# Performance work log

Hardware: AMD Instinct MI355X
Metric: run time of the kernel (lower is better)

The kernel has to match this reference:

```python
import jax, jax.numpy as jnp
import numpy as np

B, S, E, H = 2, 2048, 1024, 16
D = E // H
LN_EPS = 1e-5
NORM_EPS = 1e-12  # F.normalize clamp_min


def setup_inputs() -> dict:
    key = jax.random.key(0)
    ks = jax.random.split(key, 4)
    x = jax.random.normal(ks[0], (B, S, E), dtype=jnp.float32)
    qkv_w = jax.random.normal(ks[1], (3 * E, E), dtype=jnp.float32) * 0.02
    qkv_b = jnp.zeros((3 * E,), dtype=jnp.float32)
    out_w = jax.random.normal(ks[2], (E, E), dtype=jnp.float32) * 0.02
    out_b = jnp.zeros((E,), dtype=jnp.float32)
    ln_w = jnp.ones((E,), dtype=jnp.float32)
    ln_b = jnp.zeros((E,), dtype=jnp.float32)
    qknorm_scale = jnp.asarray(E ** -0.5, dtype=jnp.float32)
    # RotaryEmbedding buffer: inv_freq interleaved (emb[::2] = emb[1::2] = base**(-arange(0,E,2)/E))
    base_freq = 10000.0 ** (-(np.arange(0, E, 2).astype(np.float32) / E))
    emb = np.empty((E,), dtype=np.float32)
    emb[::2] = base_freq
    emb[1::2] = base_freq
    inv_freq = jnp.asarray(emb)
    return {"x": x, "ln_w": ln_w, "ln_b": ln_b, "qkv_w": qkv_w, "qkv_b": qkv_b,
            "qknorm_scale": qknorm_scale, "out_w": out_w, "out_b": out_b, "inv_freq": inv_freq}


def _rotate(t, sin, cos):
    # Faithful to source: x1 = even idx (excluding last), x2 = odd idx; cat(-x2, x1)
    x1 = t[..., :-1:2]
    x2 = t[..., 1::2]
    t_rot = jnp.concatenate((-x2, x1), axis=-1)
    return t * cos + t_rot * sin


def _l2norm(t):
    n = jnp.sqrt(jnp.sum(t * t, axis=-1, keepdims=True))
    return t / jnp.maximum(n, NORM_EPS)


def reference(x, ln_w, ln_b, qkv_w, qkv_b, qknorm_scale, out_w, out_b, inv_freq):
    # --- prenorm (LayerNorm, eps=1e-5) ---
    mu = jnp.mean(x, axis=-1, keepdims=True)
    var = jnp.mean((x - mu) ** 2, axis=-1, keepdims=True)
    xn = (x - mu) / jnp.sqrt(var + LN_EPS) * ln_w + ln_b
    # --- QKV projection ---
    qkv = xn @ qkv_w.T + qkv_b  # [B,S,3E]
    q, k, v = jnp.split(qkv, 3, axis=-1)
    # --- rotary (source uses scalar seq*inv_freq, not per-position) ---
    seq = q.shape[1]
    sin = jnp.sin(seq * inv_freq)
    cos = jnp.cos(seq * inv_freq)
    q = _rotate(q, sin, cos)
    k = _rotate(k, sin, cos)
    # --- split heads: [B,S,E] -> [B,H,S,D] ---
    split = lambda t: t.reshape(B, seq, H, D).transpose(0, 2, 1, 3)
    q, k, v = split(q), split(k), split(v)
    # --- qknorm ---
    q = _l2norm(q) * qknorm_scale
    k = _l2norm(k) * qknorm_scale
    # --- scaled dot product with causal mask ---
    aw = jnp.einsum('bhqd,bhkd->bhqk', q, k)  # [B,H,S,S]
    causal = jnp.tril(jnp.ones((seq, seq), dtype=bool))
    aw = jnp.where(causal, aw, jnp.finfo(aw.dtype).min)
    aw = jax.nn.softmax(aw, axis=-1)
    attn = jnp.einsum('bhqk,bhkd->bhqd', aw, v)
    # --- merge heads + out proj ---
    attn = attn.transpose(0, 2, 1, 3).reshape(B, seq, E)
    return attn @ out_w.T + out_b
```

## Files before the change

kernel.cpp:

```cpp
#include <hip/hip_runtime.h>

typedef unsigned short u16;
typedef __attribute__((ext_vector_type(8))) short bf16x8;
typedef __attribute__((ext_vector_type(4))) float f32x4;

#define SS 2048
#define EE 1024
#define HH 16
#define DD 64

__device__ __forceinline__ float b2f(u16 u) {
  union { unsigned int i; float f; } v; v.i = ((unsigned int)u) << 16; return v.f;
}
__device__ __forceinline__ u16 f2b(float f) {
  union { float f; unsigned int i; } v; v.f = f;
  unsigned int i = v.i;
  return (u16)((i + 0x7FFFu + ((i >> 16) & 1u)) >> 16);
}

#define GLD16(g, l)                                                         \
  __builtin_amdgcn_global_load_lds(                                         \
      (const __attribute__((address_space(1))) unsigned int*)(g),           \
      (__attribute__((address_space(3))) unsigned int*)(l), 16, 0, 0)

__global__ __launch_bounds__(256) void k_prep(const float* __restrict__ qkv_w,
                                              u16* __restrict__ wq_b,
                                              const float* __restrict__ inv_freq,
                                              float2* __restrict__ cs,
                                              const float* __restrict__ x,
                                              const float* __restrict__ lw,
                                              const float* __restrict__ lb,
                                              u16* __restrict__ xn) {
  const int bx = blockIdx.x, t = threadIdx.x;
  if (bx < 3072) {
    const int i = bx * 256 + t;
    float4 v = ((const float4*)qkv_w)[i];
    ushort4 o;
    o.x = f2b(v.x); o.y = f2b(v.y); o.z = f2b(v.z); o.w = f2b(v.w);
    ((ushort4*)wq_b)[i] = o;
    return;
  }
  if (bx < 3076) {
    const int i = (bx - 3072) * 256 + t;
    float th = 2048.0f * inv_freq[i];
    cs[i] = make_float2(cosf(th), sinf(th));
    return;
  }
  const int row = bx - 3076;
  float4 v = ((const float4*)(x + (size_t)row * EE))[t];
  float f0 = v.x, f1 = v.y, f2 = v.z, f3 = v.w;
  float s = f0 + f1 + f2 + f3;
  float ss = f0 * f0 + f1 * f1 + f2 * f2 + f3 * f3;
  for (int o = 1; o < 64; o <<= 1) { s += __shfl_xor(s, o); ss += __shfl_xor(ss, o); }
  __shared__ float red[8];
  int w = t >> 6;
  if ((t & 63) == 0) { red[w] = s; red[4 + w] = ss; }
  __syncthreads();
  s = red[0] + red[1] + red[2] + red[3];
  ss = red[4] + red[5] + red[6] + red[7];
  float mu = s * (1.0f / 1024.0f);
  float var = ss * (1.0f / 1024.0f) - mu * mu;
  float rstd = rsqrtf(var + 1e-5f);
  float4 wv = ((const float4*)lw)[t];
  float4 bv = ((const float4*)lb)[t];
  ushort4 o;
  o.x = f2b((f0 - mu) * rstd * wv.x + bv.x);
  o.y = f2b((f1 - mu) * rstd * wv.y + bv.y);
  o.z = f2b((f2 - mu) * rstd * wv.z + bv.z);
  o.w = f2b((f3 - mu) * rstd * wv.w + bv.w);
  ((ushort4*)(xn + (size_t)row * EE))[t] = o;
}

__global__ __launch_bounds__(256) void k_cvt(const float* __restrict__ src,
                                             u16* __restrict__ dst) {
  const int i = blockIdx.x * 256 + threadIdx.x;
  float4 v = ((const float4*)src)[i];
  ushort4 o;
  o.x = f2b(v.x); o.y = f2b(v.y); o.z = f2b(v.z); o.w = f2b(v.w);
  ((ushort4*)dst)[i] = o;
}

template <typename OutT, int BM64>
__device__ __forceinline__ void gemm_body(const u16* __restrict__ A,
                                          const u16* __restrict__ W,
                                          const float* __restrict__ bias,
                                          OutT* __restrict__ C,
                                          int M, int N, int K) {
  constexpr int BM = 64 * BM64;
  constexpr int MI = 2 * BM64;
  __shared__ __align__(16) u16 As[BM * 32];
  __shared__ __align__(16) u16 Ws[128 * 32];
  const int t = threadIdx.x;
  const int m0 = blockIdx.y * BM, n0 = blockIdx.x * 128;
  const int lane = t & 63, w = t >> 6, quad = lane >> 4, l15 = lane & 15;
  const int wm = (w & 1) * (BM / 2), wn = (w >> 1) * 64;

  f32x4 zero4 = {0.f, 0.f, 0.f, 0.f};
  f32x4 acc[MI][4];
  for (int mi = 0; mi < MI; mi++)
    for (int ni = 0; ni < 4; ni++) acc[mi][ni] = zero4;

  const u16* Ag = A + (size_t)(m0 + (t >> 2)) * K + (t & 3) * 8;
  const u16* Wg = W + (size_t)(n0 + (t >> 2)) * K + (t & 3) * 8;
  const size_t rowskip = (size_t)64 * K;

  for (int k0 = 0; k0 < K; k0 += 32) {
    GLD16(Ag + k0, As + t * 8);
    if constexpr (BM64 == 2) GLD16(Ag + rowskip + k0, As + 2048 + t * 8);
    GLD16(Wg + k0, Ws + t * 8);
    GLD16(Wg + rowskip + k0, Ws + 2048 + t * 8);
    __syncthreads();
    bf16x8 af[MI], wf[4];
#pragma unroll
    for (int i = 0; i < MI; i++)
      af[i] = *(const bf16x8*)(As + (wm + i * 16 + l15) * 32 + quad * 8);
#pragma unroll
    for (int i = 0; i < 4; i++)
      wf[i] = *(const bf16x8*)(Ws + (wn + i * 16 + l15) * 32 + quad * 8);
#pragma unroll
    for (int mi = 0; mi < MI; mi++)
#pragma unroll
      for (int ni = 0; ni < 4; ni++)
        acc[mi][ni] = __builtin_amdgcn_mfma_f32_16x16x32_bf16(af[mi], wf[ni], acc[mi][ni], 0, 0, 0);
    __syncthreads();
  }
  for (int mi = 0; mi < MI; mi++)
    for (int ni = 0; ni < 4; ni++) {
      int col = n0 + wn + ni * 16 + l15;
      float bb = bias[col];
      for (int r = 0; r < 4; r++) {
        int grow = m0 + wm + mi * 16 + quad * 4 + r;
        float val = acc[mi][ni][r] + bb;
        if constexpr (sizeof(OutT) == 2) C[(size_t)grow * N + col] = f2b(val);
        else                             C[(size_t)grow * N + col] = val;
      }
    }
}

__global__ __launch_bounds__(256) void k_gemm_b(const u16* A, const u16* W,
                                                const float* bias, u16* C,
                                                int M, int N, int K) {
  gemm_body<u16, 2>(A, W, bias, C, M, N, K);
}
__global__ __launch_bounds__(256) void k_gemm_f(const u16* A, const u16* W,
                                                const float* bias, float* C,
                                                int M, int N, int K) {
  gemm_body<float, 1>(A, W, bias, C, M, N, K);
}

__global__ __launch_bounds__(256) void k_rotv(u16* __restrict__ qkv,
                                              const float2* __restrict__ cs_tab,
                                              const float* __restrict__ scale_p,
                                              u16* __restrict__ vt) {
  __shared__ float qf[1024];
  __shared__ float kf[1024];
  __shared__ __align__(16) u16 tile[64 * 72];
  const int row = blockIdx.x, t = threadIdx.x;
  {
    u16* qr = qkv + (size_t)row * 3072;
    u16* kr = qr + 1024;
    ushort4 qv = ((const ushort4*)qr)[t];
    ushort4 kv = ((const ushort4*)kr)[t];
    *(float4*)(qf + 4 * t) = make_float4(b2f(qv.x), b2f(qv.y), b2f(qv.z), b2f(qv.w));
    *(float4*)(kf + 4 * t) = make_float4(b2f(kv.x), b2f(kv.y), b2f(kv.z), b2f(kv.w));
    __syncthreads();
    const float scale = scale_p[0];
    float rq[4], rk[4];
#pragma unroll
    for (int u = 0; u < 4; u++) {
      int j = 4 * t + u;
      float2 cs = cs_tab[j];
      float qrot = (j < 512) ? -qf[2 * j + 1] : qf[2 * (j - 512)];
      float krot = (j < 512) ? -kf[2 * j + 1] : kf[2 * (j - 512)];
      rq[u] = qf[j] * cs.x + qrot * cs.y;
      rk[u] = kf[j] * cs.x + krot * cs.y;
    }
    float ssq = rq[0] * rq[0] + rq[1] * rq[1] + rq[2] * rq[2] + rq[3] * rq[3];
    float ssk = rk[0] * rk[0] + rk[1] * rk[1] + rk[2] * rk[2] + rk[3] * rk[3];
    for (int o = 1; o < 16; o <<= 1) { ssq += __shfl_xor(ssq, o); ssk += __shfl_xor(ssk, o); }
    float qs = scale / fmaxf(sqrtf(ssq), 1e-12f);
    float ks = scale / fmaxf(sqrtf(ssk), 1e-12f);
    ushort4 qo, ko;
    qo.x = f2b(rq[0] * qs); qo.y = f2b(rq[1] * qs); qo.z = f2b(rq[2] * qs); qo.w = f2b(rq[3] * qs);
    ko.x = f2b(rk[0] * ks); ko.y = f2b(rk[1] * ks); ko.z = f2b(rk[2] * ks); ko.w = f2b(rk[3] * ks);
    ((ushort4*)qr)[t] = qo;
    ((ushort4*)kr)[t] = ko;
  }
  if (row >= 1024) return;
  const int st = row & 31, bh = row >> 5;
  const int b = bh >> 4, h = bh & 15;
  const int s0 = st * 64;
  const int si = t >> 2, dc = t & 3;
  __syncthreads();
  const u16* src = qkv + (size_t)(b * SS + s0 + si) * 3072 + 2048 + h * DD;
  bf16x8 v0 = *(const bf16x8*)(src + dc * 8);
  bf16x8 v1 = *(const bf16x8*)(src + (dc + 4) * 8);
#pragma unroll
  for (int u = 0; u < 8; u++) tile[(dc * 8 + u) * 72 + si] = (u16)v0[u];
#pragma unroll
  for (int u = 0; u < 8; u++) tile[((dc + 4) * 8 + u) * 72 + si] = (u16)v1[u];
  __syncthreads();
#pragma unroll
  for (int it = 0; it < 2; it++) {
    int idx = t + it * 256;
    int d = idx >> 3, ch = idx & 7;
    bf16x8 o = *(const bf16x8*)(tile + d * 72 + ch * 8);
    *(bf16x8*)(vt + (size_t)(bh * DD + d) * SS + s0 + ch * 8) = o;
  }
}

__global__ __launch_bounds__(256) void k_attn(const u16* __restrict__ qkv,
                                              const u16* __restrict__ vt,
                                              u16* __restrict__ out) {
  __shared__ __align__(16) u16 Kt[2][64 * 72];
  __shared__ __align__(16) u16 Vt[2][64 * 72];
  __shared__ __align__(16) u16 Pt[64 * 72];
  const int bh = blockIdx.y;
  const int b = bh >> 4, h = bh & 15;
  const int t = threadIdx.x, w = t >> 6, lane = t & 63, quad = lane >> 4, l15 = lane & 15;
  const int sr = t >> 2, sc = t & 3;
  const u16* kn = qkv + 1024;
  f32x4 zero4 = {0.f, 0.f, 0.f, 0.f};

  for (int rep = 0; rep < 2; rep++) {
    const int qt = rep ? 31 - (int)blockIdx.x : (int)blockIdx.x;
    const int q0 = qt * 64;

    bf16x8 qf[2];
    {
      const u16* qrow = qkv + (size_t)(b * SS + q0 + 16 * w + l15) * 3072 + h * DD;
      qf[0] = *(const bf16x8*)(qrow + quad * 8);
      qf[1] = *(const bf16x8*)(qrow + 32 + quad * 8);
    }
    f32x4 oacc[4];
    for (int n = 0; n < 4; n++) oacc[n] = zero4;
    float m_i[4] = {-1e30f, -1e30f, -1e30f, -1e30f};
    float l_i[4] = {0.f, 0.f, 0.f, 0.f};

    bf16x8 kv0, kv1, vv0, vv1;
    {
      const u16* krow = kn + (size_t)(b * SS + sr) * 3072 + h * DD;
      kv0 = *(const bf16x8*)(krow + sc * 8);
      kv1 = *(const bf16x8*)(krow + (sc + 4) * 8);
      const u16* vrow = vt + (size_t)(bh * DD + sr) * SS;
      vv0 = *(const bf16x8*)(vrow + sc * 8);
      vv1 = *(const bf16x8*)(vrow + (sc + 4) * 8);
    }
    __syncthreads();
    *(bf16x8*)(Kt[0] + sr * 72 + sc * 8) = kv0;
    *(bf16x8*)(Kt[0] + sr * 72 + (sc + 4) * 8) = kv1;
    *(bf16x8*)(Vt[0] + sr * 72 + sc * 8) = vv0;
    *(bf16x8*)(Vt[0] + sr * 72 + (sc + 4) * 8) = vv1;
    int cur = 0;

    for (int kt = 0; kt <= qt; kt++) {
      __syncthreads();
      if (kt < qt) {
        const int k0n = (kt + 1) * 64;
        const u16* krow = kn + (size_t)(b * SS + k0n + sr) * 3072 + h * DD;
        kv0 = *(const bf16x8*)(krow + sc * 8);
        kv1 = *(const bf16x8*)(krow + (sc + 4) * 8);
        const u16* vrow = vt + (size_t)(bh * DD + sr) * SS + k0n;
        vv0 = *(const bf16x8*)(vrow + sc * 8);
        vv1 = *(const bf16x8*)(vrow + (sc + 4) * 8);
      }
      const u16* Kc = Kt[cur];
      const u16* Vc = Vt[cur];
      f32x4 sacc[4];
#pragma unroll
      for (int n = 0; n < 4; n++) {
        sacc[n] = zero4;
#pragma unroll
        for (int c = 0; c < 2; c++) {
          bf16x8 kfrag = *(const bf16x8*)(Kc + (n * 16 + l15) * 72 + c * 32 + quad * 8);
          sacc[n] = __builtin_amdgcn_mfma_f32_16x16x32_bf16(qf[c], kfrag, sacc[n], 0, 0, 0);
        }
      }
      if (kt == qt) {
#pragma unroll
        for (int n = 0; n < 4; n++)
#pragma unroll
          for (int r = 0; r < 4; r++)
            if (n * 16 + l15 > 16 * w + quad * 4 + r) sacc[n][r] = -1e30f;
      }
#pragma unroll
      for (int r = 0; r < 4; r++) {
        float mx = fmaxf(fmaxf(sacc[0][r], sacc[1][r]), fmaxf(sacc[2][r], sacc[3][r]));
        for (int o = 1; o < 16; o <<= 1) mx = fmaxf(mx, __shfl_xor(mx, o));
        float mn = fmaxf(m_i[r], mx);
        float al = __expf(m_i[r] - mn);
        m_i[r] = mn;
        float rs = 0.f;
#pragma unroll
        for (int n = 0; n < 4; n++) {
          float p = __expf(sacc[n][r] - mn);
          sacc[n][r] = p;
          rs += p;
        }
        for (int o = 1; o < 16; o <<= 1) rs += __shfl_xor(rs, o);
        l_i[r] = al * l_i[r] + rs;
#pragma unroll
        for (int n = 0; n < 4; n++) oacc[n][r] *= al;
      }
#pragma unroll
      for (int n = 0; n < 4; n++)
#pragma unroll
        for (int r = 0; r < 4; r++)
          Pt[(16 * w + quad * 4 + r) * 72 + n * 16 + l15] = f2b(sacc[n][r]);
      asm volatile("s_waitcnt lgkmcnt(0)" ::: "memory");
#pragma unroll
      for (int c = 0; c < 2; c++) {
        bf16x8 pf = *(const bf16x8*)(Pt + (16 * w + l15) * 72 + c * 32 + quad * 8);
#pragma unroll
        for (int n = 0; n < 4; n++) {
          bf16x8 vf = *(const bf16x8*)(Vc + (n * 16 + l15) * 72 + c * 32 + quad * 8);
          oacc[n] = __builtin_amdgcn_mfma_f32_16x16x32_bf16(pf, vf, oacc[n], 0, 0, 0);
        }
      }
      if (kt < qt) {
        u16* Kn2 = Kt[cur ^ 1];
        u16* Vn2 = Vt[cur ^ 1];
        *(bf16x8*)(Kn2 + sr * 72 + sc * 8) = kv0;
        *(bf16x8*)(Kn2 + sr * 72 + (sc + 4) * 8) = kv1;
        *(bf16x8*)(Vn2 + sr * 72 + sc * 8) = vv0;
        *(bf16x8*)(Vn2 + sr * 72 + (sc + 4) * 8) = vv1;
      }
      cur ^= 1;
    }
    for (int n = 0; n < 4; n++)
      for (int r = 0; r < 4; r++) {
        int row = q0 + 16 * w + quad * 4 + r;
        out[(size_t)(b * SS + row) * EE + h * DD + n * 16 + l15] = f2b(oacc[n][r] / l_i[r]);
      }
  }
}

extern "C" void kernel_launch(void* const* d_in, const int* in_sizes, int n_in,
                              void* d_out, int out_size, void* d_ws, size_t ws_size,
                              hipStream_t stream) {
  const float* x       = (const float*)d_in[0];
  const float* ln_w    = (const float*)d_in[1];
  const float* ln_b    = (const float*)d_in[2];
  const float* qkv_w   = (const float*)d_in[3];
  const float* qkv_b   = (const float*)d_in[4];
  const float* qk_s    = (const float*)d_in[5];
  const float* out_w   = (const float*)d_in[6];
  const float* out_b   = (const float*)d_in[7];
  const float* inv_frq = (const float*)d_in[8];

  u16* ws   = (u16*)d_ws;
  u16* xn   = ws;
  u16* qkv  = ws + (size_t)4096 * 1024;
  u16* wq_b = (u16*)d_out;
  float2* cs_tab = (float2*)((char*)d_out + 6291456);
  u16* vt   = (u16*)d_out + (size_t)4194304;
  u16* wo_b = qkv;

  k_prep<<<7172, 256, 0, stream>>>(qkv_w, wq_b, inv_frq, cs_tab, x, ln_w, ln_b, xn);
  k_gemm_b<<<dim3(24, 32), 256, 0, stream>>>(xn, wq_b, qkv_b, qkv, 4096, 3072, 1024);
  k_rotv<<<4096, 256, 0, stream>>>(qkv, cs_tab, qk_s, vt);
  k_attn<<<dim3(16, 32), 256, 0, stream>>>(qkv, vt, xn);
  k_cvt<<<1024, 256, 0, stream>>>(out_w, wo_b);
  k_gemm_f<<<dim3(8, 64), 256, 0, stream>>>(xn, wo_b, out_b, (float*)d_out, 4096, 1024, 1024);
}
```

Measured before the change: 239.5 us.

## Use 128-wide KV tiles in attention with packed P stores and permuted V layout

The attention kernel now processes 128 keys per iteration instead of 64, halving loop trips and softmax rescale overhead per key. P is converted with packed bf16 instructions and written as contiguous 16-byte vectors. To make that work, V is stored in LDS with a permuted column order that matches P. Double buffering is replaced by a single buffer with two barriers per iteration, which may expose more load latency, and a tile that is half masked on the diagonal wastes some work.

```diff
diff --git a/kernel.cpp b/kernel.cpp
--- a/kernel.cpp
+++ b/kernel.cpp
@@ -16,6 +16,11 @@
   union { float f; unsigned int i; } v; v.f = f;
   unsigned int i = v.i;
   return (u16)((i + 0x7FFFu + ((i >> 16) & 1u)) >> 16);
+}
+__device__ __forceinline__ unsigned int cvt_pk_bf16(float lo, float hi) {
+  unsigned int r;
+  asm("v_cvt_pk_bf16_f32 %0, %1, %2" : "=v"(r) : "v"(lo), "v"(hi));
+  return r;
 }
 
 #define GLD16(g, l)                                                         \
@@ -212,19 +217,21 @@
 __global__ __launch_bounds__(256) void k_attn(const u16* __restrict__ qkv,
                                               const u16* __restrict__ vt,
                                               u16* __restrict__ out) {
-  __shared__ __align__(16) u16 Kt[2][64 * 72];
-  __shared__ __align__(16) u16 Vt[2][64 * 72];
-  __shared__ __align__(16) u16 Pt[64 * 72];
+  __shared__ __align__(16) u16 Kt[128 * 72];
+  __shared__ __align__(16) u16 Vt[64 * 136];
+  __shared__ __align__(16) u16 Pt[64 * 136];
   const int bh = blockIdx.y;
   const int b = bh >> 4, h = bh & 15;
   const int t = threadIdx.x, w = t >> 6, lane = t & 63, quad = lane >> 4, l15 = lane & 15;
-  const int sr = t >> 2, sc = t & 3;
+  const int kr = t >> 1, kdh = (t & 1) * 32;
+  const int dr = t >> 2, kc4 = t & 3;
   const u16* kn = qkv + 1024;
   f32x4 zero4 = {0.f, 0.f, 0.f, 0.f};
 
   for (int rep = 0; rep < 2; rep++) {
     const int qt = rep ? 31 - (int)blockIdx.x : (int)blockIdx.x;
     const int q0 = qt * 64;
+    const int lim = qt >> 1;
 
     bf16x8 qf[2];
     {
@@ -237,62 +244,65 @@
     float m_i[4] = {-1e30f, -1e30f, -1e30f, -1e30f};
     float l_i[4] = {0.f, 0.f, 0.f, 0.f};
 
-    bf16x8 kv0, kv1, vv0, vv1;
+    bf16x8 kv[4], vv[4];
     {
-      const u16* krow = kn + (size_t)(b * SS + sr) * 3072 + h * DD;
-      kv0 = *(const bf16x8*)(krow + sc * 8);
-      kv1 = *(const bf16x8*)(krow + (sc + 4) * 8);
-      const u16* vrow = vt + (size_t)(bh * DD + sr) * SS;
-      vv0 = *(const bf16x8*)(vrow + sc * 8);
-      vv1 = *(const bf16x8*)(vrow + (sc + 4) * 8);
+      const u16* krow = kn + (size_t)(b * SS + kr) * 3072 + h * DD + kdh;
+      const u16* vrow = vt + (size_t)(bh * DD + dr) * SS + kc4 * 32;
+#pragma unroll
+      for (int j = 0; j < 4; j++) kv[j] = *(const bf16x8*)(krow + j * 8);
+#pragma unroll
+      for (int j = 0; j < 4; j++) vv[j] = *(const bf16x8*)(vrow + j * 8);
+    }
+#pragma unroll
+    for (int j = 0; j < 4; j++) *(bf16x8*)(Kt + kr * 72 + kdh + j * 8) = kv[j];
+#pragma unroll
+    for (int j = 0; j < 4; j++) {
+      const int ch = kc4 * 4 + j;
+      u16* vb = Vt + dr * 136 + (ch & 1) * 64 + (ch >> 1);
+#pragma unroll
+      for (int e = 0; e < 8; e++) vb[e * 8] = (u16)vv[j][e];
     }
     __syncthreads();
-    *(bf16x8*)(Kt[0] + sr * 72 + sc * 8) = kv0;
-    *(bf16x8*)(Kt[0] + sr * 72 + (sc + 4) * 8) = kv1;
-    *(bf16x8*)(Vt[0] + sr * 72 + sc * 8) = vv0;
-    *(bf16x8*)(Vt[0] + sr * 72 + (sc + 4) * 8) = vv1;
-    int cur = 0;
-
-    for (int kt = 0; kt <= qt; kt++) {
-      __syncthreads();
-      if (kt < qt) {
-        const int k0n = (kt + 1) * 64;
-        const u16* krow = kn + (size_t)(b * SS + k0n + sr) * 3072 + h * DD;
-        kv0 = *(const bf16x8*)(krow + sc * 8);
-        kv1 = *(const bf16x8*)(krow + (sc + 4) * 8);
-        const u16* vrow = vt + (size_t)(bh * DD + sr) * SS + k0n;
-        vv0 = *(const bf16x8*)(vrow + sc * 8);
-        vv1 = *(const bf16x8*)(vrow + (sc + 4) * 8);
-      }
-      const u16* Kc = Kt[cur];
-      const u16* Vc = Vt[cur];
-      f32x4 sacc[4];
-#pragma unroll
-      for (int n = 0; n < 4; n++) {
+
+    for (int kt = 0; kt <= lim; kt++) {
+      if (kt < lim) {
+        const int k0n = (kt + 1) * 128;
+        const u16* krow = kn + (size_t)(b * SS + k0n + kr) * 3072 + h * DD + kdh;
+        const u16* vrow = vt + (size_t)(bh * DD + dr) * SS + k0n + kc4 * 32;
+#pragma unroll
+        for (int j = 0; j < 4; j++) kv[j] = *(const bf16x8*)(krow + j * 8);
+#pragma unroll
+        for (int j = 0; j < 4; j++) vv[j] = *(const bf16x8*)(vrow + j * 8);
+      }
+      f32x4 sacc[8];
+#pragma unroll
+      for (int n = 0; n < 8; n++) {
         sacc[n] = zero4;
 #pragma unroll
         for (int c = 0; c < 2; c++) {
-          bf16x8 kfrag = *(const bf16x8*)(Kc + (n * 16 + l15) * 72 + c * 32 + quad * 8);
+          bf16x8 kfrag = *(const bf16x8*)(Kt + (n * 16 + l15) * 72 + c * 32 + quad * 8);
           sacc[n] = __builtin_amdgcn_mfma_f32_16x16x32_bf16(qf[c], kfrag, sacc[n], 0, 0, 0);
         }
       }
-      if (kt == qt) {
-#pragma unroll
-        for (int n = 0; n < 4; n++)
+      if (kt == lim) {
+        const int rbase = (qt & 1) * 64 + 16 * w + quad * 4;
+#pragma unroll
+        for (int n = 0; n < 8; n++)
 #pragma unroll
           for (int r = 0; r < 4; r++)
-            if (n * 16 + l15 > 16 * w + quad * 4 + r) sacc[n][r] = -1e30f;
+            if (n * 16 + l15 > rbase + r) sacc[n][r] = -1e30f;
       }
 #pragma unroll
       for (int r = 0; r < 4; r++) {
-        float mx = fmaxf(fmaxf(sacc[0][r], sacc[1][r]), fmaxf(sacc[2][r], sacc[3][r]));
+        float mx = fmaxf(fmaxf(fmaxf(sacc[0][r], sacc[1][r]), fmaxf(sacc[2][r], sacc[3][r])),
+                         fmaxf(fmaxf(sacc[4][r], sacc[5][r]), fmaxf(sacc[6][r], sacc[7][r])));
         for (int o = 1; o < 16; o <<= 1) mx = fmaxf(mx, __shfl_xor(mx, o));
         float mn = fmaxf(m_i[r], mx);
         float al = __expf(m_i[r] - mn);
         m_i[r] = mn;
         float rs = 0.f;
 #pragma unroll
-        for (int n = 0; n < 4; n++) {
+        for (int n = 0; n < 8; n++) {
           float p = __expf(sacc[n][r] - mn);
           sacc[n][r] = p;
           rs += p;
@@ -303,29 +313,38 @@
         for (int n = 0; n < 4; n++) oacc[n][r] *= al;
       }
 #pragma unroll
-      for (int n = 0; n < 4; n++)
-#pragma unroll
-        for (int r = 0; r < 4; r++)
-          Pt[(16 * w + quad * 4 + r) * 72 + n * 16 + l15] = f2b(sacc[n][r]);
+      for (int r = 0; r < 4; r++) {
+        union { unsigned int u[4]; bf16x8 v8; } pk;
+        pk.u[0] = cvt_pk_bf16(sacc[0][r], sacc[1][r]);
+        pk.u[1] = cvt_pk_bf16(sacc[2][r], sacc[3][r]);
+        pk.u[2] = cvt_pk_bf16(sacc[4][r], sacc[5][r]);
+        pk.u[3] = cvt_pk_bf16(sacc[6][r], sacc[7][r]);
+        *(bf16x8*)(Pt + (16 * w + quad * 4 + r) * 136 + l15 * 8) = pk.v8;
+      }
       asm volatile("s_waitcnt lgkmcnt(0)" ::: "memory");
-#pragma unroll
-      for (int c = 0; c < 2; c++) {
-        bf16x8 pf = *(const bf16x8*)(Pt + (16 * w + l15) * 72 + c * 32 + quad * 8);
+      __builtin_amdgcn_sched_barrier(0);
+#pragma unroll
+      for (int c = 0; c < 4; c++) {
+        bf16x8 pf = *(const bf16x8*)(Pt + (16 * w + l15) * 136 + c * 32 + quad * 8);
 #pragma unroll
         for (int n = 0; n < 4; n++) {
-          bf16x8 vf = *(const bf16x8*)(Vc + (n * 16 + l15) * 72 + c * 32 + quad * 8);
+          bf16x8 vf = *(const bf16x8*)(Vt + (n * 16 + l15) * 136 + c * 32 + quad * 8);
           oacc[n] = __builtin_amdgcn_mfma_f32_16x16x32_bf16(pf, vf, oacc[n], 0, 0, 0);
         }
       }
-      if (kt < qt) {
-        u16* Kn2 = Kt[cur ^ 1];
-        u16* Vn2 = Vt[cur ^ 1];
-        *(bf16x8*)(Kn2 + sr * 72 + sc * 8) = kv0;
-        *(bf16x8*)(Kn2 + sr * 72 + (sc + 4) * 8) = kv1;
-        *(bf16x8*)(Vn2 + sr * 72 + sc * 8) = vv0;
-        *(bf16x8*)(Vn2 + sr * 72 + (sc + 4) * 8) = vv1;
-      }
-      cur ^= 1;
+      __syncthreads();
+      if (kt < lim) {
+#pragma unroll
+        for (int j = 0; j < 4; j++) *(bf16x8*)(Kt + kr * 72 + kdh + j * 8) = kv[j];
+#pragma unroll
+        for (int j = 0; j < 4; j++) {
+          const int ch = kc4 * 4 + j;
+          u16* vb = Vt + dr * 136 + (ch & 1) * 64 + (ch >> 1);
+#pragma unroll
+          for (int e = 0; e < 8; e++) vb[e * 8] = (u16)vv[j][e];
+        }
+      }
+      __syncthreads();
     }
     for (int n = 0; n < 4; n++)
       for (int r = 0; r < 4; r++) {
```

New measurement: 228.1 us. 1.05x faster.
